# Kernel tuning notes

Hardware: AMD Instinct MI355X
Metric: run time of the kernel (lower is better)

The kernel has to match this reference:

```python
import jax, jax.numpy as jnp
import numpy as np

N_NODES = 100000
N_EDGES = 1600000
D = 128
NEG_SLOPE = 0.01  # torch F.leaky_relu default


def setup_inputs() -> dict:
    key = jax.random.key(0)
    k1, k2, k3, k4, k5 = jax.random.split(key, 5)
    nfeat = jax.random.normal(k1, (N_NODES, D), dtype=jnp.float32)
    edge_src = jax.random.randint(k2, (N_EDGES,), 0, N_NODES, dtype=jnp.int32)
    edge_dst = jax.random.randint(k3, (N_EDGES,), 0, N_NODES, dtype=jnp.int32)
    edge_w = jax.random.uniform(k4, (N_EDGES,), dtype=jnp.float32)
    W = jax.random.normal(k5, (D, D), dtype=jnp.float32) * (1.0 / np.sqrt(D))
    return {"nfeat": nfeat, "edge_src": edge_src, "edge_dst": edge_dst,
            "edge_w": edge_w, "W": W}


def reference(nfeat, edge_src, edge_dst, edge_w, W):
    # message: m_e = h[src_e] * w_e  (u_mul_e)
    msg = nfeat[edge_src] * edge_w[:, None]          # [E, D]
    # reduce: h_neighbor[v] = sum_{e: dst(e)=v} m_e  (fn.sum)
    h_neighbor = jax.ops.segment_sum(msg, edge_dst, num_segments=nfeat.shape[0])  # [N, D]
    # Bi-interaction residual: leaky_relu(Linear(h * h_neighbor)); dropout = identity (eval)
    out = jax.nn.leaky_relu((nfeat * h_neighbor) @ W.T, negative_slope=NEG_SLOPE)
    return out
```

## Files before the change

kernel.cpp:

```cpp
#include <hip/hip_runtime.h>
#include <hip/hip_fp16.h>

#define NNODES 100000
#define NEDGES 1600000
#define DIM    128
#define NEG_SLOPE 0.01f
#define NB_SCAN ((NNODES + 1023) / 1024)
#define NPART 8
#define PART_SZ ((NNODES + NPART - 1) / NPART)
#define NSUB 64
#define SUB_SZ ((NNODES + NSUB - 1) / NSUB)
#define SCAP 27000
#define SCUR_STRIDE 32
#define CHUNK 2048
#define GEMM_TILES ((NNODES + 63) / 64)

typedef _Float16     v8h __attribute__((ext_vector_type(8)));
typedef float        v4f __attribute__((ext_vector_type(4)));
typedef int          v4i __attribute__((ext_vector_type(4)));
typedef int          v2i __attribute__((ext_vector_type(2)));
typedef float        v4x __attribute__((ext_vector_type(4)));
typedef unsigned int v2u __attribute__((ext_vector_type(2)));
typedef unsigned int v4u __attribute__((ext_vector_type(4)));

static inline size_t align256(size_t x) { return (x + 255) & ~(size_t)255; }

union HU { unsigned int u; __half2 h; };

__global__ __launch_bounds__(256) void zero_f32(float* __restrict__ p, int n4) {
    int i = blockIdx.x * blockDim.x + threadIdx.x;
    int stride = gridDim.x * blockDim.x;
    float4 z = make_float4(0.f, 0.f, 0.f, 0.f);
    for (; i < n4; i += stride) ((float4*)p)[i] = z;
}

__global__ __launch_bounds__(256) void prep(const float* __restrict__ nf,
                                            const float* __restrict__ W,
                                            __half* __restrict__ nf16,
                                            __half* __restrict__ W16,
                                            int* __restrict__ counts,
                                            int* __restrict__ scur) {
    int i = blockIdx.x * 256 + threadIdx.x;
    int stride = gridDim.x * 256;
    for (int j = i; j < NNODES * DIM / 4; j += stride) {
        v4x v = __builtin_nontemporal_load((const v4x*)nf + j);
        HU a, b;
        a.h = __float22half2_rn(make_float2(v.x, v.y));
        b.h = __float22half2_rn(make_float2(v.z, v.w));
        ((uint2*)nf16)[j] = make_uint2(a.u, b.u);
    }
    const float4* Wg4 = (const float4*)W;
    for (int j = i; j < DIM * DIM / 8; j += stride) {
        float4 lo = Wg4[j * 2], hi = Wg4[j * 2 + 1];
        HU a, b, c, d;
        a.h = __float22half2_rn(make_float2(lo.x, lo.y));
        b.h = __float22half2_rn(make_float2(lo.z, lo.w));
        c.h = __float22half2_rn(make_float2(hi.x, hi.y));
        d.h = __float22half2_rn(make_float2(hi.z, hi.w));
        ((uint4*)W16)[j] = make_uint4(a.u, b.u, c.u, d.u);
    }
    v4i z = (v4i){0, 0, 0, 0};
    for (int j = i; j < NNODES / 4; j += stride)
        *((v4i*)counts + j) = z;
    if (i < NSUB * SCUR_STRIDE) scur[i] = 0;
}

__global__ __launch_bounds__(256) void split_edges(const int* __restrict__ esrc,
                                                   const int* __restrict__ edst,
                                                   const float* __restrict__ ew,
                                                   int* __restrict__ scur,
                                                   int2* __restrict__ pairs) {
    __shared__ int wcnt[4][NSUB];
    __shared__ int wbase[4][NSUB];
    __shared__ int gbase[NSUB];
    int tid = threadIdx.x;
    int wave = tid >> 6;
    ((int*)wcnt)[tid] = 0;
    __syncthreads();

    int nq = NEDGES / 4;
    int qA = blockIdx.x * (CHUNK / 4) + tid;
    int qB = qA + 256;

    v4i dA = (v4i){0,0,0,0}, sA = (v4i){0,0,0,0};
    v4x wA = (v4x){0,0,0,0};
    v4i dB = (v4i){0,0,0,0}, sB = (v4i){0,0,0,0};
    v4x wB = (v4x){0,0,0,0};
    bool vA = qA < nq, vB = qB < nq;
    if (vA) {
        dA = __builtin_nontemporal_load((const v4i*)edst + qA);
        sA = __builtin_nontemporal_load((const v4i*)esrc + qA);
        wA = __builtin_nontemporal_load((const v4x*)ew + qA);
    }
    if (vB) {
        dB = __builtin_nontemporal_load((const v4i*)edst + qB);
        sB = __builtin_nontemporal_load((const v4i*)esrc + qB);
        wB = __builtin_nontemporal_load((const v4x*)ew + qB);
    }

    int sp8[8]; int rnk[8]; int2 pv[8];
    #pragma unroll
    for (int k = 0; k < 4; ++k) {
        int d = dA[k], s = sA[k];
        int p = vA ? (int)((unsigned)d / SUB_SZ) : -1;
        sp8[k] = p;
        pv[k] = make_int2(((d - p * SUB_SZ) << 17) | s, __float_as_int(wA[k]));
        int d2 = dB[k], s2 = sB[k];
        int p2 = vB ? (int)((unsigned)d2 / SUB_SZ) : -1;
        sp8[k + 4] = p2;
        pv[k + 4] = make_int2(((d2 - p2 * SUB_SZ) << 17) | s2, __float_as_int(wB[k]));
    }

    #pragma unroll
    for (int s = 0; s < 8; ++s) {
        if (sp8[s] >= 0)
            rnk[s] = atomicAdd(&wcnt[wave][sp8[s]], 1);
    }
    __syncthreads();
    if (tid < NSUB) {
        int t0 = wcnt[0][tid], t1 = wcnt[1][tid], t2 = wcnt[2][tid], t3 = wcnt[3][tid];
        wbase[0][tid] = 0; wbase[1][tid] = t0;
        wbase[2][tid] = t0 + t1; wbase[3][tid] = t0 + t1 + t2;
        gbase[tid] = atomicAdd(&scur[tid * SCUR_STRIDE], t0 + t1 + t2 + t3);
    }
    __syncthreads();

    #pragma unroll
    for (int s = 0; s < 8; ++s) {
        int p = sp8[s];
        if (p >= 0) {
            int slot = gbase[p] + wbase[wave][p] + rnk[s];
            if (slot < SCAP)
                pairs[(size_t)p * SCAP + slot] = pv[s];
        }
    }
}

__global__ __launch_bounds__(256) void hist_part(const int2* __restrict__ pairs,
                                                 const int* __restrict__ scur,
                                                 int* __restrict__ counts) {
    int b = blockIdx.x;
    int sp = b & 63;
    int w = b >> 6;
    int n = scur[sp * SCUR_STRIDE];
    if (n > SCAP) n = SCAP;
    const int2* base = pairs + (size_t)sp * SCAP;
    int cbase = sp * SUB_SZ;
    int ng = n >> 2;
    for (int i = w * 256 + threadIdx.x; i < ng; i += 8192) {
        v4i a = __builtin_nontemporal_load((const v4i*)base + 2 * i);
        v4i c = __builtin_nontemporal_load((const v4i*)base + 2 * i + 1);
        atomicAdd(&counts[cbase + ((unsigned)a.x >> 17)], 1);
        atomicAdd(&counts[cbase + ((unsigned)a.z >> 17)], 1);
        atomicAdd(&counts[cbase + ((unsigned)c.x >> 17)], 1);
        atomicAdd(&counts[cbase + ((unsigned)c.z >> 17)], 1);
    }
    if (w == 0 && threadIdx.x < 3) {
        int idx = (ng << 2) + threadIdx.x;
        if (idx < n) {
            int2 pr = base[idx];
            atomicAdd(&counts[cbase + ((unsigned)pr.x >> 17)], 1);
        }
    }
}

__global__ __launch_bounds__(256) void scan1(const int* __restrict__ counts,
                                             int* __restrict__ offsets,
                                             int* __restrict__ blocksum) {
    __shared__ int lds[256];
    int tid = threadIdx.x;
    int base = blockIdx.x * 1024 + tid * 4;
    int c0 = (base + 0 < NNODES) ? counts[base + 0] : 0;
    int c1 = (base + 1 < NNODES) ? counts[base + 1] : 0;
    int c2 = (base + 2 < NNODES) ? counts[base + 2] : 0;
    int c3 = (base + 3 < NNODES) ? counts[base + 3] : 0;
    int t = c0 + c1 + c2 + c3;
    lds[tid] = t;
    __syncthreads();
    for (int d = 1; d < 256; d <<= 1) {
        int v = lds[tid];
        int add = (tid >= d) ? lds[tid - d] : 0;
        __syncthreads();
        lds[tid] = v + add;
        __syncthreads();
    }
    int incl = lds[tid];
    int excl = incl - t;
    if (base + 0 < NNODES) offsets[base + 0] = excl;
    if (base + 1 < NNODES) offsets[base + 1] = excl + c0;
    if (base + 2 < NNODES) offsets[base + 2] = excl + c0 + c1;
    if (base + 3 < NNODES) offsets[base + 3] = excl + c0 + c1 + c2;
    if (tid == 255) blocksum[blockIdx.x] = incl;
}

__global__ __launch_bounds__(128) void scan2p(int* __restrict__ blocksum, int nb) {
    __shared__ int lds[128];
    int tid = threadIdx.x;
    int v = (tid < nb) ? blocksum[tid] : 0;
    lds[tid] = v;
    __syncthreads();
    for (int d = 1; d < 128; d <<= 1) {
        int x = lds[tid];
        int add = (tid >= d) ? lds[tid - d] : 0;
        __syncthreads();
        lds[tid] = x + add;
        __syncthreads();
    }
    if (tid < nb) blocksum[tid] = lds[tid] - v;
}

__global__ __launch_bounds__(256) void scan3(int* __restrict__ offsets,
                                             const int* __restrict__ blocksum) {
    int add = blocksum[blockIdx.x];
    int base = blockIdx.x * 1024 + threadIdx.x * 4;
    #pragma unroll
    for (int i = 0; i < 4; ++i) {
        int idx = base + i;
        if (idx < NNODES) offsets[idx] += add;
    }
}

__global__ __launch_bounds__(256) void fill_part2(const int2* __restrict__ pairs,
                                                  const int* __restrict__ scur,
                                                  int* __restrict__ offsets,
                                                  int2* __restrict__ bins) {
    int b = blockIdx.x;
    int sp = b & 63;
    int w = b >> 6;
    int n = scur[sp * SCUR_STRIDE];
    if (n > SCAP) n = SCAP;
    const int2* base = pairs + (size_t)sp * SCAP;
    int cbase = sp * SUB_SZ;
    int ng = n >> 2;
    for (int i = w * 256 + threadIdx.x; i < ng; i += 8192) {
        v4i a = __builtin_nontemporal_load((const v4i*)base + 2 * i);
        v4i c = __builtin_nontemporal_load((const v4i*)base + 2 * i + 1);
        int d0 = cbase + ((unsigned)a.x >> 17);
        int p0 = atomicAdd(&offsets[d0], 1);
        bins[p0] = make_int2(a.x & 0x1FFFF, a.y);
        int d1 = cbase + ((unsigned)a.z >> 17);
        int p1 = atomicAdd(&offsets[d1], 1);
        bins[p1] = make_int2(a.z & 0x1FFFF, a.w);
        int d2 = cbase + ((unsigned)c.x >> 17);
        int p2 = atomicAdd(&offsets[d2], 1);
        bins[p2] = make_int2(c.x & 0x1FFFF, c.y);
        int d3 = cbase + ((unsigned)c.z >> 17);
        int p3 = atomicAdd(&offsets[d3], 1);
        bins[p3] = make_int2(c.z & 0x1FFFF, c.w);
    }
    if (w == 0 && threadIdx.x < 3) {
        int idx = (ng << 2) + threadIdx.x;
        if (idx < n) {
            int2 pr = base[idx];
            int d = cbase + ((unsigned)pr.x >> 17);
            int p = atomicAdd(&offsets[d], 1);
            bins[p] = make_int2(pr.x & 0x1FFFF, pr.y);
        }
    }
}

__global__ __launch_bounds__(256) void pull_x16(const __half* __restrict__ nf16,
                                                const int* __restrict__ offsets,
                                                const int* __restrict__ counts,
                                                const int2* __restrict__ bins,
                                                __half* __restrict__ x16) {
    int gid = blockIdx.x * 256 + threadIdx.x;
    int v = gid >> 5;
    int lane = gid & 31;
    if (v >= NNODES) return;
    int end = offsets[v];
    int start = end - counts[v];
    const uint2* nf2 = (const uint2*)nf16;
    float4 a0 = make_float4(0.f, 0.f, 0.f, 0.f);
    float4 a1 = make_float4(0.f, 0.f, 0.f, 0.f);
    float4 a2 = make_float4(0.f, 0.f, 0.f, 0.f);
    float4 a3 = make_float4(0.f, 0.f, 0.f, 0.f);
    int k = start;
    for (; k + 4 <= end; k += 4) {
        v2i e0 = __builtin_nontemporal_load((const v2i*)bins + k);
        v2i e1 = __builtin_nontemporal_load((const v2i*)bins + k + 1);
        v2i e2 = __builtin_nontemporal_load((const v2i*)bins + k + 2);
        v2i e3 = __builtin_nontemporal_load((const v2i*)bins + k + 3);
        uint2 u0 = nf2[(size_t)e0.x * 32 + lane];
        uint2 u1 = nf2[(size_t)e1.x * 32 + lane];
        uint2 u2 = nf2[(size_t)e2.x * 32 + lane];
        uint2 u3 = nf2[(size_t)e3.x * 32 + lane];
        float w0 = __int_as_float(e0.y), w1 = __int_as_float(e1.y);
        float w2 = __int_as_float(e2.y), w3 = __int_as_float(e3.y);
        HU h; float2 f;
        h.u = u0.x; f = __half22float2(h.h); a0.x += w0 * f.x; a0.y += w0 * f.y;
        h.u = u0.y; f = __half22float2(h.h); a0.z += w0 * f.x; a0.w += w0 * f.y;
        h.u = u1.x; f = __half22float2(h.h); a1.x += w1 * f.x; a1.y += w1 * f.y;
        h.u = u1.y; f = __half22float2(h.h); a1.z += w1 * f.x; a1.w += w1 * f.y;
        h.u = u2.x; f = __half22float2(h.h); a2.x += w2 * f.x; a2.y += w2 * f.y;
        h.u = u2.y; f = __half22float2(h.h); a2.z += w2 * f.x; a2.w += w2 * f.y;
        h.u = u3.x; f = __half22float2(h.h); a3.x += w3 * f.x; a3.y += w3 * f.y;
        h.u = u3.y; f = __half22float2(h.h); a3.z += w3 * f.x; a3.w += w3 * f.y;
    }
    for (; k < end; ++k) {
        v2i e = __builtin_nontemporal_load((const v2i*)bins + k);
        float w = __int_as_float(e.y);
        uint2 u = nf2[(size_t)e.x * 32 + lane];
        HU h; float2 f;
        h.u = u.x; f = __half22float2(h.h); a0.x += w * f.x; a0.y += w * f.y;
        h.u = u.y; f = __half22float2(h.h); a0.z += w * f.x; a0.w += w * f.y;
    }
    float4 acc;
    acc.x = (a0.x + a1.x) + (a2.x + a3.x);
    acc.y = (a0.y + a1.y) + (a2.y + a3.y);
    acc.z = (a0.z + a1.z) + (a2.z + a3.z);
    acc.w = (a0.w + a1.w) + (a2.w + a3.w);
    uint2 un = nf2[(size_t)v * 32 + lane];
    HU h; float2 f;
    h.u = un.x; f = __half22float2(h.h); acc.x *= f.x; acc.y *= f.y;
    h.u = un.y; f = __half22float2(h.h); acc.z *= f.x; acc.w *= f.y;
    HU o0, o1;
    o0.h = __float22half2_rn(make_float2(acc.x, acc.y));
    o1.h = __float22half2_rn(make_float2(acc.z, acc.w));
    v2u ov = (v2u){o0.u, o1.u};
    __builtin_nontemporal_store(ov, (v2u*)x16 + (size_t)v * 32 + lane);
}

__global__ __launch_bounds__(256) void gemm16(const __half* __restrict__ x16,
                                              const __half* __restrict__ W16,
                                              float* __restrict__ out) {
    __shared__ _Float16 Wl[128 * 128];
    __shared__ _Float16 Xl[64 * 128];
    int tid = threadIdx.x;

    const v4u* Wg = (const v4u*)W16;
    for (int i = tid; i < 2048; i += 256) {
        int r = i >> 4, c = i & 15;
        v4u u = Wg[i];
        *(v4u*)&Wl[r * 128 + ((c ^ (r & 7)) << 3)] = u;
    }

    int rbase = blockIdx.x * 64;
    for (int i = tid; i < 1024; i += 256) {
        int r = i >> 4, c = i & 15;
        int grow = rbase + r;
        v4u u = (v4u){0u, 0u, 0u, 0u};
        if (grow < NNODES)
            u = __builtin_nontemporal_load((const v4u*)x16 + (size_t)grow * 16 + c);
        *(v4u*)&Xl[r * 128 + ((c ^ (r & 7)) << 3)] = u;
    }
    __syncthreads();

    int wave = tid >> 6;
    int lane = tid & 63;
    int n = lane & 15;
    int g = lane >> 4;

    v4f acc[8];
    #pragma unroll
    for (int jb = 0; jb < 8; ++jb) acc[jb] = (v4f){0.f, 0.f, 0.f, 0.f};

    #pragma unroll
    for (int kb = 0; kb < 4; ++kb) {
        v8h a = *(v8h*)&Xl[(wave * 16 + n) * 128 + (((kb * 4 + g) ^ (n & 7)) << 3)];
        #pragma unroll
        for (int jb = 0; jb < 8; ++jb) {
            v8h b = *(v8h*)&Wl[(jb * 16 + n) * 128 + (((kb * 4 + g) ^ (n & 7)) << 3)];
            acc[jb] = __builtin_amdgcn_mfma_f32_16x16x32_f16(a, b, acc[jb], 0, 0, 0);
        }
    }

    int row0 = rbase + wave * 16 + g * 4;
    #pragma unroll
    for (int jb = 0; jb < 8; ++jb) {
        #pragma unroll
        for (int reg = 0; reg < 4; ++reg) {
            int r = row0 + reg;
            if (r < NNODES) {
                float v = acc[jb][reg];
                v = v >= 0.f ? v : NEG_SLOPE * v;
                __builtin_nontemporal_store(v, out + (size_t)r * 128 + jb * 16 + n);
            }
        }
    }
}

__global__ __launch_bounds__(256) void hist_dst4(const int* __restrict__ edst,
                                                 int* __restrict__ counts) {
    int i = blockIdx.x * 256 + threadIdx.x;
    if (i < NEDGES / 4) {
        int4 d = ((const int4*)edst)[i];
        atomicAdd(&counts[d.x], 1);
        atomicAdd(&counts[d.y], 1);
        atomicAdd(&counts[d.z], 1);
        atomicAdd(&counts[d.w], 1);
    }
}

__global__ __launch_bounds__(256) void fill_part(const int* __restrict__ esrc,
                                                 const int* __restrict__ edst,
                                                 const float* __restrict__ ew,
                                                 int* __restrict__ offsets,
                                                 int2* __restrict__ bins) {
    int part = blockIdx.x & (NPART - 1);
    int lo = part * PART_SZ;
    int hi = lo + PART_SZ;
    int t = (blockIdx.x >> 3) * 256 + threadIdx.x;
    int stride = (gridDim.x >> 3) * 256;
    int nq = NEDGES / 4;
    for (int i = t; i < nq; i += stride) {
        int4 d = ((const int4*)edst)[i];
        int e = i * 4;
        if (d.x >= lo && d.x < hi) {
            int p = atomicAdd(&offsets[d.x], 1);
            bins[p] = make_int2(esrc[e + 0], __float_as_int(ew[e + 0]));
        }
        if (d.y >= lo && d.y < hi) {
            int p = atomicAdd(&offsets[d.y], 1);
            bins[p] = make_int2(esrc[e + 1], __float_as_int(ew[e + 1]));
        }
        if (d.z >= lo && d.z < hi) {
            int p = atomicAdd(&offsets[d.z], 1);
            bins[p] = make_int2(esrc[e + 2], __float_as_int(ew[e + 2]));
        }
        if (d.w >= lo && d.w < hi) {
            int p = atomicAdd(&offsets[d.w], 1);
            bins[p] = make_int2(esrc[e + 3], __float_as_int(ew[e + 3]));
        }
    }
}

__global__ __launch_bounds__(256) void scatter_edges(
    const float* __restrict__ nfeat, const int* __restrict__ esrc,
    const int* __restrict__ edst, const float* __restrict__ ew,
    float* __restrict__ hn) {
    long long t = (long long)blockIdx.x * 256 + threadIdx.x;
    int e = (int)(t >> 5);
    if (e >= NEDGES) return;
    int lane = (int)(t & 31);
    int s = esrc[e];
    int d = edst[e];
    float w = ew[e];
    float4 v = ((const float4*)(nfeat + (size_t)s * DIM))[lane];
    float* o = hn + (size_t)d * DIM + lane * 4;
    unsafeAtomicAdd(o + 0, v.x * w);
    unsafeAtomicAdd(o + 1, v.y * w);
    unsafeAtomicAdd(o + 2, v.z * w);
    unsafeAtomicAdd(o + 3, v.w * w);
}

__global__ __launch_bounds__(256) void elem_mul(const float* __restrict__ nfeat,
                                                float* __restrict__ hn, int n4) {
    int i = blockIdx.x * blockDim.x + threadIdx.x;
    int stride = gridDim.x * blockDim.x;
    for (; i < n4; i += stride) {
        float4 a = ((const float4*)nfeat)[i];
        float4 b = ((float4*)hn)[i];
        b.x *= a.x; b.y *= a.y; b.z *= a.z; b.w *= a.w;
        ((float4*)hn)[i] = b;
    }
}

__global__ __launch_bounds__(256) void bi_gemm2(
    const float* __restrict__ x, const float* __restrict__ W,
    float* __restrict__ out) {
    extern __shared__ float lds[];
    float4* W4  = (float4*)lds;
    float*  xs  = lds + 128 * 128;
    float4* xs4 = (float4*)xs;
    int tid = threadIdx.x;
    const float4* Wg = (const float4*)W;
    for (int i = tid; i < 128 * 32; i += 256) {
        int j = i >> 5, d4 = i & 31;
        W4[(j << 5) | (d4 ^ ((j >> 2) & 7))] = Wg[i];
    }
    __syncthreads();
    int tx = tid & 31, ty = tid >> 5;
    int j0 = tx << 2, r0 = ty << 2;
    int ntiles = NNODES / 32;
    for (int tile = blockIdx.x; tile < ntiles; tile += gridDim.x) {
        int rbase = tile * 32;
        for (int i = tid; i < 32 * 32; i += 256)
            xs4[i] = ((const float4*)x)[(size_t)rbase * 32 + i];
        __syncthreads();
        float acc[4][4];
        #pragma unroll
        for (int r = 0; r < 4; ++r)
            #pragma unroll
            for (int j = 0; j < 4; ++j) acc[r][j] = 0.f;
        #pragma unroll 4
        for (int d4 = 0; d4 < 32; ++d4) {
            float4 xv[4], wv[4];
            #pragma unroll
            for (int r = 0; r < 4; ++r) xv[r] = xs4[((r0 + r) << 5) | d4];
            #pragma unroll
            for (int j = 0; j < 4; ++j) {
                int jj = j0 + j;
                wv[j] = W4[(jj << 5) | (d4 ^ ((jj >> 2) & 7))];
            }
            #pragma unroll
            for (int r = 0; r < 4; ++r)
                #pragma unroll
                for (int j = 0; j < 4; ++j) {
                    acc[r][j] += xv[r].x * wv[j].x;
                    acc[r][j] += xv[r].y * wv[j].y;
                    acc[r][j] += xv[r].z * wv[j].z;
                    acc[r][j] += xv[r].w * wv[j].w;
                }
        }
        __syncthreads();
        #pragma unroll
        for (int r = 0; r < 4; ++r) {
            float4 o;
            o.x = acc[r][0] >= 0.f ? acc[r][0] : NEG_SLOPE * acc[r][0];
            o.y = acc[r][1] >= 0.f ? acc[r][1] : NEG_SLOPE * acc[r][1];
            o.z = acc[r][2] >= 0.f ? acc[r][2] : NEG_SLOPE * acc[r][2];
            o.w = acc[r][3] >= 0.f ? acc[r][3] : NEG_SLOPE * acc[r][3];
            size_t row = (size_t)(rbase + r0 + r);
            ((float4*)out)[row * (DIM / 4) + tx] = o;
        }
    }
}

extern "C" void kernel_launch(void* const* d_in, const int* in_sizes, int n_in,
                              void* d_out, int out_size, void* d_ws, size_t ws_size,
                              hipStream_t stream) {
    const float* nfeat = (const float*)d_in[0];
    const int*   esrc  = (const int*)d_in[1];
    const int*   edst  = (const int*)d_in[2];
    const float* ew    = (const float*)d_in[3];
    const float* W     = (const float*)d_in[4];
    float* out = (float*)d_out;

    size_t off = 0;
    size_t nf16_off = off;     off += align256((size_t)NNODES * DIM * 2);
    size_t x16_off = off;      off += align256((size_t)NNODES * DIM * 2);
    size_t w16_off = off;      off += align256((size_t)DIM * DIM * 2);
    size_t cnt_off = off;      off += align256((size_t)NNODES * 4);
    size_t ofs_off = off;      off += align256((size_t)NNODES * 4);
    size_t scur_off = off;     off += align256((size_t)NSUB * SCUR_STRIDE * 4);
    size_t bsum_off = off;     off += align256((size_t)NB_SCAN * 4);
    size_t bins_off = off;     off += align256((size_t)NEDGES * 8);
    size_t need_mid = off;
    size_t pair_off = off;     off += align256((size_t)NSUB * SCAP * 8);
    size_t need_full = off;

    char* ws = (char*)d_ws;

    if (ws_size >= need_mid) {
        __half* nf16 = (__half*)(ws + nf16_off);
        __half* x16  = (__half*)(ws + x16_off);
        __half* W16  = (__half*)(ws + w16_off);
        int* counts = (int*)(ws + cnt_off);
        int* offsets = (int*)(ws + ofs_off);
        int* scur = (int*)(ws + scur_off);
        int* blocksum = (int*)(ws + bsum_off);
        int2* bins = (int2*)(ws + bins_off);
        int2* pairs = (int2*)(ws + pair_off);

        prep<<<2048, 256, 0, stream>>>(nfeat, W, nf16, W16, counts, scur);
        if (ws_size >= need_full) {
            int sgrid = (NEDGES + CHUNK - 1) / CHUNK;
            split_edges<<<sgrid, 256, 0, stream>>>(esrc, edst, ew, scur, pairs);
            hist_part<<<2048, 256, 0, stream>>>(pairs, scur, counts);
            scan1<<<NB_SCAN, 256, 0, stream>>>(counts, offsets, blocksum);
            scan2p<<<1, 128, 0, stream>>>(blocksum, NB_SCAN);
            scan3<<<NB_SCAN, 256, 0, stream>>>(offsets, blocksum);
            fill_part2<<<2048, 256, 0, stream>>>(pairs, scur, offsets, bins);
        } else {
            int e4grid = (NEDGES / 4 + 255) / 256;
            hist_dst4<<<e4grid, 256, 0, stream>>>(edst, counts);
            scan1<<<NB_SCAN, 256, 0, stream>>>(counts, offsets, blocksum);
            scan2p<<<1, 128, 0, stream>>>(blocksum, NB_SCAN);
            scan3<<<NB_SCAN, 256, 0, stream>>>(offsets, blocksum);
            fill_part<<<2048, 256, 0, stream>>>(esrc, edst, ew, offsets, bins);
        }
        int pgrid = (NNODES * 32 + 255) / 256;
        pull_x16<<<pgrid, 256, 0, stream>>>(nf16, offsets, counts, bins, x16);
        gemm16<<<GEMM_TILES, 256, 0, stream>>>(x16, W16, out);
    } else {
        float* hn = (float*)ws;
        hipFuncSetAttribute((const void*)bi_gemm2,
                            hipFuncAttributeMaxDynamicSharedMemorySize, 81920);
        zero_f32<<<2048, 256, 0, stream>>>(hn, NNODES * DIM / 4);
        int sgrid = (NEDGES * 32 + 255) / 256;
        scatter_edges<<<sgrid, 256, 0, stream>>>(nfeat, esrc, edst, ew, hn);
        elem_mul<<<2048, 256, 0, stream>>>(nfeat, hn, NNODES * DIM / 4);
        bi_gemm2<<<512, 256, 81920, stream>>>(hn, W, out);
    }
}
```

Baseline: 251.0 us.

## Fuse prep conversion into split_edges and merge scan phases two and three

Moves the fp16 conversion of node features and W, plus the zeroing of counts, into the tail of split_edges so that one launch does both jobs. The scur zeroing becomes a hipMemsetAsync. scan2p and scan3 are merged into scan23, where every block redundantly scans the block sums in LDS and applies its own offset. This removes two launches and their gaps, but split_edges now does more work per block, and every scan block repeats the small block-sum scan.

```diff
diff --git a/kernel.cpp b/kernel.cpp
--- a/kernel.cpp
+++ b/kernel.cpp
@@ -38,8 +38,7 @@
                                             const float* __restrict__ W,
                                             __half* __restrict__ nf16,
                                             __half* __restrict__ W16,
-                                            int* __restrict__ counts,
-                                            int* __restrict__ scur) {
+                                            int* __restrict__ counts) {
     int i = blockIdx.x * 256 + threadIdx.x;
     int stride = gridDim.x * 256;
     for (int j = i; j < NNODES * DIM / 4; j += stride) {
@@ -62,14 +61,18 @@
     v4i z = (v4i){0, 0, 0, 0};
     for (int j = i; j < NNODES / 4; j += stride)
         *((v4i*)counts + j) = z;
-    if (i < NSUB * SCUR_STRIDE) scur[i] = 0;
 }
 
 __global__ __launch_bounds__(256) void split_edges(const int* __restrict__ esrc,
                                                    const int* __restrict__ edst,
                                                    const float* __restrict__ ew,
                                                    int* __restrict__ scur,
-                                                   int2* __restrict__ pairs) {
+                                                   int2* __restrict__ pairs,
+                                                   const float* __restrict__ nf,
+                                                   const float* __restrict__ W,
+                                                   __half* __restrict__ nf16,
+                                                   __half* __restrict__ W16,
+                                                   int* __restrict__ counts) {
     __shared__ int wcnt[4][NSUB];
     __shared__ int wbase[4][NSUB];
     __shared__ int gbase[NSUB];
@@ -134,6 +137,29 @@
                 pairs[(size_t)p * SCAP + slot] = pv[s];
         }
     }
+
+    int gi = blockIdx.x * 256 + tid;
+    int gstride = gridDim.x * 256;
+    for (int j = gi; j < NNODES * DIM / 4; j += gstride) {
+        v4x v = __builtin_nontemporal_load((const v4x*)nf + j);
+        HU a, b;
+        a.h = __float22half2_rn(make_float2(v.x, v.y));
+        b.h = __float22half2_rn(make_float2(v.z, v.w));
+        ((uint2*)nf16)[j] = make_uint2(a.u, b.u);
+    }
+    const float4* Wg4 = (const float4*)W;
+    for (int j = gi; j < DIM * DIM / 8; j += gstride) {
+        float4 lo = Wg4[j * 2], hi = Wg4[j * 2 + 1];
+        HU a, b, c, d;
+        a.h = __float22half2_rn(make_float2(lo.x, lo.y));
+        b.h = __float22half2_rn(make_float2(lo.z, lo.w));
+        c.h = __float22half2_rn(make_float2(hi.x, hi.y));
+        d.h = __float22half2_rn(make_float2(hi.z, hi.w));
+        ((uint4*)W16)[j] = make_uint4(a.u, b.u, c.u, d.u);
+    }
+    v4i z = (v4i){0, 0, 0, 0};
+    for (int j = gi; j < NNODES / 4; j += gstride)
+        *((v4i*)counts + j) = z;
 }
 
 __global__ __launch_bounds__(256) void hist_part(const int2* __restrict__ pairs,
@@ -193,26 +219,21 @@
     if (tid == 255) blocksum[blockIdx.x] = incl;
 }
 
-__global__ __launch_bounds__(128) void scan2p(int* __restrict__ blocksum, int nb) {
+__global__ __launch_bounds__(256) void scan23(int* __restrict__ offsets,
+                                              const int* __restrict__ blocksum) {
     __shared__ int lds[128];
     int tid = threadIdx.x;
-    int v = (tid < nb) ? blocksum[tid] : 0;
-    lds[tid] = v;
+    if (tid < 128) lds[tid] = (tid < NB_SCAN) ? blocksum[tid] : 0;
     __syncthreads();
     for (int d = 1; d < 128; d <<= 1) {
-        int x = lds[tid];
-        int add = (tid >= d) ? lds[tid - d] : 0;
+        int x = (tid < 128) ? lds[tid] : 0;
+        int addv = (tid >= d && tid < 128) ? lds[tid - d] : 0;
         __syncthreads();
-        lds[tid] = x + add;
+        if (tid < 128) lds[tid] = x + addv;
         __syncthreads();
     }
-    if (tid < nb) blocksum[tid] = lds[tid] - v;
-}
-
-__global__ __launch_bounds__(256) void scan3(int* __restrict__ offsets,
-                                             const int* __restrict__ blocksum) {
-    int add = blocksum[blockIdx.x];
-    int base = blockIdx.x * 1024 + threadIdx.x * 4;
+    int add = (blockIdx.x == 0) ? 0 : lds[blockIdx.x - 1];
+    int base = blockIdx.x * 1024 + tid * 4;
     #pragma unroll
     for (int i = 0; i < 4; ++i) {
         int idx = base + i;
@@ -553,21 +574,21 @@
         int2* bins = (int2*)(ws + bins_off);
         int2* pairs = (int2*)(ws + pair_off);
 
-        prep<<<2048, 256, 0, stream>>>(nfeat, W, nf16, W16, counts, scur);
         if (ws_size >= need_full) {
+            hipMemsetAsync(scur, 0, (size_t)NSUB * SCUR_STRIDE * 4, stream);
             int sgrid = (NEDGES + CHUNK - 1) / CHUNK;
-            split_edges<<<sgrid, 256, 0, stream>>>(esrc, edst, ew, scur, pairs);
+            split_edges<<<sgrid, 256, 0, stream>>>(esrc, edst, ew, scur, pairs,
+                                                   nfeat, W, nf16, W16, counts);
             hist_part<<<2048, 256, 0, stream>>>(pairs, scur, counts);
             scan1<<<NB_SCAN, 256, 0, stream>>>(counts, offsets, blocksum);
-            scan2p<<<1, 128, 0, stream>>>(blocksum, NB_SCAN);
-            scan3<<<NB_SCAN, 256, 0, stream>>>(offsets, blocksum);
+            scan23<<<NB_SCAN, 256, 0, stream>>>(offsets, blocksum);
             fill_part2<<<2048, 256, 0, stream>>>(pairs, scur, offsets, bins);
         } else {
+            prep<<<2048, 256, 0, stream>>>(nfeat, W, nf16, W16, counts);
             int e4grid = (NEDGES / 4 + 255) / 256;
             hist_dst4<<<e4grid, 256, 0, stream>>>(edst, counts);
             scan1<<<NB_SCAN, 256, 0, stream>>>(counts, offsets, blocksum);
-            scan2p<<<1, 128, 0, stream>>>(blocksum, NB_SCAN);
-            scan3<<<NB_SCAN, 256, 0, stream>>>(offsets, blocksum);
+            scan23<<<NB_SCAN, 256, 0, stream>>>(offsets, blocksum);
             fill_part<<<2048, 256, 0, stream>>>(esrc, edst, ew, offsets, bins);
         }
         int pgrid = (NNODES * 32 + 255) / 256;
```

After: 253.2 us. Within noise of the previous version (+0.9%).

## Accumulate neighbor sums in packed fp16 with 16 lanes per node; read W from global

Applied to the files above, without the earlier changes.

The pull kernel now gives each node 16 lanes that each load a uint4 (8 halves) and accumulate with packed half2 FMAs instead of converting to fp32. This halves thread count and the conversion ALU work, and widens per-lane loads. A separate single-accumulator variant serves the mid-workspace path. The GEMM stops staging W in LDS and reads B fragments straight from global/L2, cutting LDS use and setup. The fp16 accumulation of about 16 terms per node lowers precision and risks tolerance failures.

```diff
diff --git a/kernel.cpp b/kernel.cpp
--- a/kernel.cpp
+++ b/kernel.cpp
@@ -26,6 +26,7 @@
 static inline size_t align256(size_t x) { return (x + 255) & ~(size_t)255; }
 
 union HU { unsigned int u; __half2 h; };
+union U4H { uint4 u; __half2 h[4]; };
 
 __global__ __launch_bounds__(256) void zero_f32(float* __restrict__ p, int n4) {
     int i = blockIdx.x * blockDim.x + threadIdx.x;
@@ -265,75 +266,61 @@
                                                 const int2* __restrict__ bins,
                                                 __half* __restrict__ x16) {
     int gid = blockIdx.x * 256 + threadIdx.x;
-    int v = gid >> 5;
-    int lane = gid & 31;
+    int v = gid >> 4;
+    int lane = gid & 15;
     if (v >= NNODES) return;
     int end = offsets[v];
     int start = end - counts[v];
-    const uint2* nf2 = (const uint2*)nf16;
-    float4 a0 = make_float4(0.f, 0.f, 0.f, 0.f);
-    float4 a1 = make_float4(0.f, 0.f, 0.f, 0.f);
-    float4 a2 = make_float4(0.f, 0.f, 0.f, 0.f);
-    float4 a3 = make_float4(0.f, 0.f, 0.f, 0.f);
+    const uint4* nfu4 = (const uint4*)nf16;
+    __half2 z2 = __float2half2_rn(0.f);
+    U4H a0, a1, a2, a3;
+    #pragma unroll
+    for (int j = 0; j < 4; ++j) { a0.h[j] = z2; a1.h[j] = z2; a2.h[j] = z2; a3.h[j] = z2; }
     int k = start;
     for (; k + 4 <= end; k += 4) {
         v2i e0 = __builtin_nontemporal_load((const v2i*)bins + k);
         v2i e1 = __builtin_nontemporal_load((const v2i*)bins + k + 1);
         v2i e2 = __builtin_nontemporal_load((const v2i*)bins + k + 2);
         v2i e3 = __builtin_nontemporal_load((const v2i*)bins + k + 3);
-        uint2 u0 = nf2[(size_t)e0.x * 32 + lane];
-        uint2 u1 = nf2[(size_t)e1.x * 32 + lane];
-        uint2 u2 = nf2[(size_t)e2.x * 32 + lane];
-        uint2 u3 = nf2[(size_t)e3.x * 32 + lane];
-        float w0 = __int_as_float(e0.y), w1 = __int_as_float(e1.y);
-        float w2 = __int_as_float(e2.y), w3 = __int_as_float(e3.y);
-        HU h; float2 f;
-        h.u = u0.x; f = __half22float2(h.h); a0.x += w0 * f.x; a0.y += w0 * f.y;
-        h.u = u0.y; f = __half22float2(h.h); a0.z += w0 * f.x; a0.w += w0 * f.y;
-        h.u = u1.x; f = __half22float2(h.h); a1.x += w1 * f.x; a1.y += w1 * f.y;
-        h.u = u1.y; f = __half22float2(h.h); a1.z += w1 * f.x; a1.w += w1 * f.y;
-        h.u = u2.x; f = __half22float2(h.h); a2.x += w2 * f.x; a2.y += w2 * f.y;
-        h.u = u2.y; f = __half22float2(h.h); a2.z += w2 * f.x; a2.w += w2 * f.y;
-        h.u = u3.x; f = __half22float2(h.h); a3.x += w3 * f.x; a3.y += w3 * f.y;
-        h.u = u3.y; f = __half22float2(h.h); a3.z += w3 * f.x; a3.w += w3 * f.y;
+        U4H u0, u1, u2, u3;
+        u0.u = nfu4[(size_t)e0.x * 16 + lane];
+        u1.u = nfu4[(size_t)e1.x * 16 + lane];
+        u2.u = nfu4[(size_t)e2.x * 16 + lane];
+        u3.u = nfu4[(size_t)e3.x * 16 + lane];
+        __half2 w0 = __float2half2_rn(__int_as_float(e0.y));
+        __half2 w1 = __float2half2_rn(__int_as_float(e1.y));
+        __half2 w2 = __float2half2_rn(__int_as_float(e2.y));
+        __half2 w3 = __float2half2_rn(__int_as_float(e3.y));
+        #pragma unroll
+        for (int j = 0; j < 4; ++j) {
+            a0.h[j] = __hfma2(w0, u0.h[j], a0.h[j]);
+            a1.h[j] = __hfma2(w1, u1.h[j], a1.h[j]);
+            a2.h[j] = __hfma2(w2, u2.h[j], a2.h[j]);
+            a3.h[j] = __hfma2(w3, u3.h[j], a3.h[j]);
+        }
     }
     for (; k < end; ++k) {
         v2i e = __builtin_nontemporal_load((const v2i*)bins + k);
-        float w = __int_as_float(e.y);
-        uint2 u = nf2[(size_t)e.x * 32 + lane];
-        HU h; float2 f;
-        h.u = u.x; f = __half22float2(h.h); a0.x += w * f.x; a0.y += w * f.y;
-        h.u = u.y; f = __half22float2(h.h); a0.z += w * f.x; a0.w += w * f.y;
-    }
-    float4 acc;
-    acc.x = (a0.x + a1.x) + (a2.x + a3.x);
-    acc.y = (a0.y + a1.y) + (a2.y + a3.y);
-    acc.z = (a0.z + a1.z) + (a2.z + a3.z);
-    acc.w = (a0.w + a1.w) + (a2.w + a3.w);
-    uint2 un = nf2[(size_t)v * 32 + lane];
-    HU h; float2 f;
-    h.u = un.x; f = __half22float2(h.h); acc.x *= f.x; acc.y *= f.y;
-    h.u = un.y; f = __half22float2(h.h); acc.z *= f.x; acc.w *= f.y;
-    HU o0, o1;
-    o0.h = __float22half2_rn(make_float2(acc.x, acc.y));
-    o1.h = __float22half2_rn(make_float2(acc.z, acc.w));
-    v2u ov = (v2u){o0.u, o1.u};
-    __builtin_nontemporal_store(ov, (v2u*)x16 + (size_t)v * 32 + lane);
+        U4H u; u.u = nfu4[(size_t)e.x * 16 + lane];
+        __half2 w = __float2half2_rn(__int_as_float(e.y));
+        #pragma unroll
+        for (int j = 0; j < 4; ++j) a0.h[j] = __hfma2(w, u.h[j], a0.h[j]);
+    }
+    U4H s, sf;
+    sf.u = nfu4[(size_t)v * 16 + lane];
+    #pragma unroll
+    for (int j = 0; j < 4; ++j) {
+        __half2 t2 = __hadd2(__hadd2(a0.h[j], a1.h[j]), __hadd2(a2.h[j], a3.h[j]));
+        s.h[j] = __hmul2(t2, sf.h[j]);
+    }
+    __builtin_nontemporal_store(*(v4u*)&s.u, (v4u*)x16 + (size_t)v * 16 + lane);
 }
 
 __global__ __launch_bounds__(256) void gemm16(const __half* __restrict__ x16,
                                               const __half* __restrict__ W16,
                                               float* __restrict__ out) {
-    __shared__ _Float16 Wl[128 * 128];
     __shared__ _Float16 Xl[64 * 128];
     int tid = threadIdx.x;
-
-    const v4u* Wg = (const v4u*)W16;
-    for (int i = tid; i < 2048; i += 256) {
-        int r = i >> 4, c = i & 15;
-        v4u u = Wg[i];
-        *(v4u*)&Wl[r * 128 + ((c ^ (r & 7)) << 3)] = u;
-    }
 
     int rbase = blockIdx.x * 64;
     for (int i = tid; i < 1024; i += 256) {
@@ -350,6 +337,7 @@
     int lane = tid & 63;
     int n = lane & 15;
     int g = lane >> 4;
+    const v8h* w8 = (const v8h*)W16;
 
     v4f acc[8];
     #pragma unroll
@@ -360,7 +348,7 @@
         v8h a = *(v8h*)&Xl[(wave * 16 + n) * 128 + (((kb * 4 + g) ^ (n & 7)) << 3)];
         #pragma unroll
         for (int jb = 0; jb < 8; ++jb) {
-            v8h b = *(v8h*)&Wl[(jb * 16 + n) * 128 + (((kb * 4 + g) ^ (n & 7)) << 3)];
+            v8h b = w8[(jb * 16 + n) * 16 + kb * 4 + g];
             acc[jb] = __builtin_amdgcn_mfma_f32_16x16x32_f16(a, b, acc[jb], 0, 0, 0);
         }
     }
@@ -423,6 +411,36 @@
             bins[p] = make_int2(esrc[e + 3], __float_as_int(ew[e + 3]));
         }
     }
+}
+
+__global__ __launch_bounds__(256) void pull_x16_mid(const __half* __restrict__ nf16,
+                                                    const int* __restrict__ offsets,
+                                                    const int* __restrict__ counts,
+                                                    const int2* __restrict__ bins,
+                                                    __half* __restrict__ x16) {
+    int gid = blockIdx.x * 256 + threadIdx.x;
+    int v = gid >> 4;
+    int lane = gid & 15;
+    if (v >= NNODES) return;
+    int end = offsets[v];
+    int start = end - counts[v];
+    const uint4* nfu4 = (const uint4*)nf16;
+    __half2 z2 = __float2half2_rn(0.f);
+    U4H a0;
+    #pragma unroll
+    for (int j = 0; j < 4; ++j) a0.h[j] = z2;
+    for (int k = start; k < end; ++k) {
+        v2i e = __builtin_nontemporal_load((const v2i*)bins + k);
+        U4H u; u.u = nfu4[(size_t)e.x * 16 + lane];
+        __half2 w = __float2half2_rn(__int_as_float(e.y));
+        #pragma unroll
+        for (int j = 0; j < 4; ++j) a0.h[j] = __hfma2(w, u.h[j], a0.h[j]);
+    }
+    U4H s, sf;
+    sf.u = nfu4[(size_t)v * 16 + lane];
+    #pragma unroll
+    for (int j = 0; j < 4; ++j) s.h[j] = __hmul2(a0.h[j], sf.h[j]);
+    __builtin_nontemporal_store(*(v4u*)&s.u, (v4u*)x16 + (size_t)v * 16 + lane);
 }
 
 __global__ __launch_bounds__(256) void scatter_edges(
@@ -554,6 +572,7 @@
         int2* pairs = (int2*)(ws + pair_off);
 
         prep<<<2048, 256, 0, stream>>>(nfeat, W, nf16, W16, counts, scur);
+        int pgrid = (NNODES * 16 + 255) / 256;
         if (ws_size >= need_full) {
             int sgrid = (NEDGES + CHUNK - 1) / CHUNK;
             split_edges<<<sgrid, 256, 0, stream>>>(esrc, edst, ew, scur, pairs);
@@ -562,6 +581,7 @@
             scan2p<<<1, 128, 0, stream>>>(blocksum, NB_SCAN);
             scan3<<<NB_SCAN, 256, 0, stream>>>(offsets, blocksum);
             fill_part2<<<2048, 256, 0, stream>>>(pairs, scur, offsets, bins);
+            pull_x16<<<pgrid, 256, 0, stream>>>(nf16, offsets, counts, bins, x16);
         } else {
             int e4grid = (NEDGES / 4 + 255) / 256;
             hist_dst4<<<e4grid, 256, 0, stream>>>(edst, counts);
@@ -569,9 +589,8 @@
             scan2p<<<1, 128, 0, stream>>>(blocksum, NB_SCAN);
             scan3<<<NB_SCAN, 256, 0, stream>>>(offsets, blocksum);
             fill_part<<<2048, 256, 0, stream>>>(esrc, edst, ew, offsets, bins);
-        }
-        int pgrid = (NNODES * 32 + 255) / 256;
-        pull_x16<<<pgrid, 256, 0, stream>>>(nf16, offsets, counts, bins, x16);
+            pull_x16_mid<<<pgrid, 256, 0, stream>>>(nf16, offsets, counts, bins, x16);
+        }
         gemm16<<<GEMM_TILES, 256, 0, stream>>>(x16, W16, out);
     } else {
         float* hn = (float*)ws;
```

Result: slower. 260.9 us (+3.9%).
